# Optimization experiments

Hardware: AMD Instinct MI355X
Metric: run time of the kernel (lower is better)

## Reference

```python
import jax, jax.numpy as jnp
import numpy as np

N = 40000      # nodes
E = 640000     # edges (avg degree 16)
H = 128        # hidden_dim
D = 4          # propagation_depth
G = 1250       # graphs in batch
T = 32         # target_dim
AF, AV = 9, 64   # atom categorical features, vocab per feature
BF, BV = 3, 8    # bond categorical features, vocab per feature


def silu(x):
    return x * jax.nn.sigmoid(x)


def setup_inputs() -> dict:
    key = jax.random.key(0)
    ks = jax.random.split(key, 32)
    s = 1.0 / np.sqrt(H)

    def w(i, shp, scale):
        return (jax.random.normal(ks[i], shp, jnp.float32) * scale).astype(jnp.float32)

    inp = {}
    inp["atom_feat"] = jax.random.randint(ks[0], (N, AF), 0, AV)
    inp["bond_feat"] = jax.random.randint(ks[1], (E, BF), 0, BV)
    inp["edge_src"] = jax.random.randint(ks[2], (E,), 0, N)
    inp["edge_dst"] = jax.random.randint(ks[3], (E,), 0, N)
    inp["node2graph"] = jnp.sort(jax.random.randint(ks[4], (N,), 0, G))

    inp["atom_emb"] = w(5, (AF, AV, H), 0.1)
    inp["bond_emb"] = w(6, (BF, BV, H), 0.1)
    # message MLP: Linear(3H,H)+SiLU, Linear(H,H)+SiLU (last_activation=mid_activation)
    inp["msg_W1"] = w(7, (D, 3 * H, H), 1.0 / np.sqrt(3 * H))
    inp["msg_b1"] = jnp.zeros((D, H), jnp.float32)
    inp["msg_W2"] = w(8, (D, H, H), s)
    inp["msg_b2"] = jnp.zeros((D, H), jnp.float32)
    # soft edge gate: Linear(H,1) + sigmoid
    inp["gate_W"] = w(9, (D, H, 1), s)
    inp["gate_b"] = jnp.zeros((D, 1), jnp.float32)
    # update MLP: Linear(H,H)+SiLU, Linear(H,H) (last None)
    inp["upd_W1"] = w(10, (D, H, H), s)
    inp["upd_b1"] = jnp.zeros((D, H), jnp.float32)
    inp["upd_W2"] = w(11, (D, H, H), s)
    inp["upd_b2"] = jnp.zeros((D, H), jnp.float32)
    # node_wise_output: Linear(H,H)+SiLU, Linear(H,H) (last None)
    inp["out_W1"] = w(12, (H, H), s)
    inp["out_b1"] = jnp.zeros((H,), jnp.float32)
    inp["out_W2"] = w(13, (H, H), s)
    inp["out_b2"] = jnp.zeros((H,), jnp.float32)
    # readout output MLP: Linear(3H,H)+ReLU, Linear(H,T) (last None)
    inp["ro_W1"] = w(14, (3 * H, H), 1.0 / np.sqrt(3 * H))
    inp["ro_b1"] = jnp.zeros((H,), jnp.float32)
    inp["ro_W2"] = w(15, (H, T), s)
    inp["ro_b2"] = jnp.zeros((T,), jnp.float32)
    return inp


def _forward(atom_feat, bond_feat, edge_src, edge_dst, node2graph,
             atom_emb, bond_emb,
             msg_W1, msg_b1, msg_W2, msg_b2, gate_W, gate_b,
             upd_W1, upd_b1, upd_W2, upd_b2,
             out_W1, out_b1, out_W2, out_b2,
             ro_W1, ro_b1, ro_W2, ro_b2):
    # Atom/Bond encoders: sum of per-feature categorical embeddings
    h = atom_emb[jnp.arange(AF), atom_feat].sum(axis=1)        # [N, H]
    e = bond_emb[jnp.arange(BF), bond_feat].sum(axis=1)        # [E, H]

    for l in range(D):
        src = h[edge_src]                                      # [E, H]
        dst = h[edge_dst]                                      # [E, H]
        m_in = jnp.concatenate([src, dst, e], axis=-1)         # [E, 3H]
        m = silu(silu(m_in @ msg_W1[l] + msg_b1[l]) @ msg_W2[l] + msg_b2[l])
        gate = jax.nn.sigmoid(m @ gate_W[l] + gate_b[l])       # [E, 1]
        m = m * gate
        m_sum = jax.ops.segment_sum(m, edge_dst, num_segments=N)  # [N, H]
        u_in = m_sum + h
        h_new = silu(u_in @ upd_W1[l] + upd_b1[l]) @ upd_W2[l] + upd_b2[l]
        h = h_new + h

    # node-wise output network
    h = silu(h @ out_W1 + out_b1) @ out_W2 + out_b2            # [N, H]

    # per-graph readouts: sum / mean / max
    sums = jax.ops.segment_sum(h, node2graph, num_segments=G)  # [G, H]
    cnt = jax.ops.segment_sum(jnp.ones((N, 1), h.dtype), node2graph, num_segments=G)
    mean = sums / jnp.maximum(cnt, 1.0)
    mx = jax.ops.segment_max(h, node2graph, num_segments=G)
    mx = jnp.where(cnt > 0, mx, 0.0)
    readout = jnp.concatenate([sums, mean, mx], axis=-1)       # [G, 3H]

    return jax.nn.relu(readout @ ro_W1 + ro_b1) @ ro_W2 + ro_b2  # [G, T]


def reference(atom_feat, bond_feat, edge_src, edge_dst, node2graph,
              atom_emb, bond_emb,
              msg_W1, msg_b1, msg_W2, msg_b2, gate_W, gate_b,
              upd_W1, upd_b1, upd_W2, upd_b2,
              out_W1, out_b1, out_W2, out_b2,
              ro_W1, ro_b1, ro_W2, ro_b2):
    return _forward(atom_feat, bond_feat, edge_src, edge_dst, node2graph,
                    atom_emb, bond_emb,
                    msg_W1, msg_b1, msg_W2, msg_b2, gate_W, gate_b,
                    upd_W1, upd_b1, upd_W2, upd_b2,
                    out_W1, out_b1, out_W2, out_b2,
                    ro_W1, ro_b1, ro_W2, ro_b2)
```

## Files before the change

kernel.cpp:

```cpp
#include <hip/hip_runtime.h>
#include <hip/hip_bf16.h>

#define NN 40000
#define NE 640000
#define HD 128
#define DEPTH 4
#define NG 1250
#define TD 32
#define AFN 9
#define AVN 64
#define BFN 3
#define BVN 8
#define NBLK (NE / 64)

typedef short bf16x8 __attribute__((ext_vector_type(8)));
typedef float f32x4 __attribute__((ext_vector_type(4)));

__device__ __forceinline__ uint cvtpk(float lo, float hi){
  uint r; asm("v_cvt_pk_bf16_f32 %0, %1, %2" : "=v"(r) : "v"(lo), "v"(hi)); return r;
}
__device__ __forceinline__ ushort f2bf(float x){
  return (ushort)cvtpk(x, x);
}
__device__ __forceinline__ float bf2f(ushort b){ return __uint_as_float(((uint)b) << 16); }
__device__ __forceinline__ float lo16f(uint w){ return __uint_as_float(w << 16); }
__device__ __forceinline__ float hi16f(uint w){ return __uint_as_float(w & 0xffff0000u); }
__device__ __forceinline__ float rcpfa(float x){ return __builtin_amdgcn_rcpf(x); }
__device__ __forceinline__ float siluf(float x){ return x * rcpfa(1.f + __expf(-x)); }
__device__ __forceinline__ float sigmf(float x){ return rcpfa(1.f + __expf(-x)); }
__device__ __forceinline__ uint packbf2(float a, float b){ return cvtpk(a, b); }

__global__ void pack_w(const float* __restrict__ src, ushort* __restrict__ dst,
                       int K, int N, int L){
  int total = L * K * N;
  for (int idx = blockIdx.x * blockDim.x + threadIdx.x; idx < total;
       idx += gridDim.x * blockDim.x){
    int l = idx / (K * N);
    int r = idx - l * K * N;
    int k = r / N;
    int n = r - k * N;
    dst[(size_t)l * K * N + ((size_t)(k >> 3) * N + n) * 8 + (k & 7)] = f2bf(src[idx]);
  }
}

__global__ void zero_f(float4* __restrict__ p, int n4){
  for (int i = blockIdx.x * blockDim.x + threadIdx.x; i < n4; i += gridDim.x * blockDim.x)
    p[i] = make_float4(0.f, 0.f, 0.f, 0.f);
}

__global__ void zero_i(int* __restrict__ p, int n){
  for (int i = blockIdx.x * blockDim.x + threadIdx.x; i < n; i += gridDim.x * blockDim.x)
    p[i] = 0;
}

__global__ void atom_encode(const int* __restrict__ feat, const float* __restrict__ emb,
                            float* __restrict__ h, ushort* __restrict__ hbf){
  int n = blockIdx.x;
  int c = threadIdx.x;
  float acc = 0.f;
#pragma unroll
  for (int f = 0; f < AFN; ++f){
    int v = feat[n * AFN + f];
    acc += emb[(size_t)(f * AVN + v) * HD + c];
  }
  h[(size_t)n * HD + c] = acc;
  hbf[(size_t)n * HD + c] = f2bf(acc);
}

__global__ void ebf_k(const float* __restrict__ bemb, ushort* __restrict__ ebf){
  const int cid = blockIdx.x;
  const int c = threadIdx.x;
  const int f0 = cid >> 6, f1 = (cid >> 3) & 7, f2 = cid & 7;
  float v = bemb[(size_t)(0 * BVN + f0) * HD + c]
          + bemb[(size_t)(1 * BVN + f1) * HD + c]
          + bemb[(size_t)(2 * BVN + f2) * HD + c];
  ebf[(size_t)cid * HD + c] = f2bf(v);
}

__global__ void hist_k(const int* __restrict__ edst, int* __restrict__ deg){
  for (int e = blockIdx.x * blockDim.x + threadIdx.x; e < NE; e += gridDim.x * blockDim.x)
    atomicAdd(&deg[edst[e]], 1);
}

__global__ __launch_bounds__(1024) void scan_head(const int* __restrict__ deg,
                                                  int* __restrict__ head){
  __shared__ int buf[1024];
  const int t = threadIdx.x;
  const int base = t * 40;
  int s = 0;
  int dloc[40];
  if (t < 1000){
#pragma unroll
    for (int i = 0; i < 40; ++i){ dloc[i] = deg[base + i]; s += dloc[i]; }
  }
  buf[t] = s;
  __syncthreads();
  for (int ofs = 1; ofs < 1024; ofs <<= 1){
    int x = (t >= ofs) ? buf[t - ofs] : 0;
    __syncthreads();
    buf[t] += x;
    __syncthreads();
  }
  if (t < 1000){
    int run = buf[t] - s;
#pragma unroll
    for (int i = 0; i < 40; ++i){ head[base + i] = run; run += dloc[i]; }
  }
}

__global__ void scatter_k(const int* __restrict__ esrc, const int* __restrict__ edst,
                          const int* __restrict__ bfeat, int* __restrict__ head,
                          int* __restrict__ esrc_p, int* __restrict__ dst_p,
                          int* __restrict__ cid_p){
  for (int e = blockIdx.x * blockDim.x + threadIdx.x; e < NE; e += gridDim.x * blockDim.x){
    const int d = edst[e];
    const int pos = atomicAdd(&head[d], 1);
    esrc_p[pos] = esrc[e];
    dst_p[pos] = d;
    cid_p[pos] = bfeat[e * 3 + 0] * 64 + bfeat[e * 3 + 1] * 8 + bfeat[e * 3 + 2];
  }
}

__global__ __launch_bounds__(256) void pre_k(
    const ushort* __restrict__ hbf, const ushort* __restrict__ W1p,
    ushort* __restrict__ prea, ushort* __restrict__ preb)
{
  const int tid = threadIdx.x;
  const int n0 = blockIdx.x * 64;
  const int lane = tid & 63, wv = tid >> 6;
  const int lr = lane & 15, lg = lane >> 4;
  const int arow = n0 + wv * 16 + lr;
  bf16x8 a[4];
#pragma unroll
  for (int ks = 0; ks < 4; ++ks)
    a[ks] = *(const bf16x8*)(hbf + (size_t)arow * HD + ks * 32 + lg * 8);
  const f32x4 zero = {0.f, 0.f, 0.f, 0.f};
  f32x4 acc[16];
#pragma unroll
  for (int i = 0; i < 16; ++i) acc[i] = zero;
#pragma unroll
  for (int ks = 0; ks < 4; ++ks){
#pragma unroll
    for (int ct = 0; ct < 16; ++ct){
      const int oct = ks * 4 + lg + ((ct >= 8) ? 16 : 0);
      const int ncol = (ct & 7) * 16 + lr;
      bf16x8 b = *(const bf16x8*)(W1p + ((size_t)oct * HD + ncol) * 8);
      acc[ct] = __builtin_amdgcn_mfma_f32_16x16x32_bf16(a[ks], b, acc[ct], 0, 0, 0);
    }
  }
#pragma unroll
  for (int ct = 0; ct < 16; ++ct){
    ushort* dstp = (ct < 8) ? prea : preb;
    const int ncol = (ct & 7) * 16 + lr;
#pragma unroll
    for (int r = 0; r < 4; ++r){
      const int nrow = n0 + wv * 16 + lg * 4 + r;
      dstp[(size_t)nrow * HD + ncol] = f2bf(acc[ct][r]);
    }
  }
}

__global__ __launch_bounds__(256) void ew1c_k(
    const ushort* __restrict__ ebf, const ushort* __restrict__ W1p_all,
    const float* __restrict__ b1_all, ushort* __restrict__ ecb_all)
{
  const int l = blockIdx.y;
  const ushort* W1p = W1p_all + (size_t)l * 384 * HD;
  const float* b1v = b1_all + l * HD;
  ushort* ecb = ecb_all + (size_t)l * 512 * HD;
  const int tid = threadIdx.x;
  const int c0 = blockIdx.x * 64;
  const int lane = tid & 63, wv = tid >> 6;
  const int lr = lane & 15, lg = lane >> 4;
  const int arow = c0 + wv * 16 + lr;
  bf16x8 a[4];
#pragma unroll
  for (int ks = 0; ks < 4; ++ks)
    a[ks] = *(const bf16x8*)(ebf + (size_t)arow * HD + ks * 32 + lg * 8);
  const f32x4 zero = {0.f, 0.f, 0.f, 0.f};
  f32x4 acc[8];
#pragma unroll
  for (int i = 0; i < 8; ++i) acc[i] = zero;
#pragma unroll
  for (int ks = 0; ks < 4; ++ks){
#pragma unroll
    for (int ct = 0; ct < 8; ++ct){
      const int oct = ks * 4 + lg + 32;
      const int ncol = ct * 16 + lr;
      bf16x8 b = *(const bf16x8*)(W1p + ((size_t)oct * HD + ncol) * 8);
      acc[ct] = __builtin_amdgcn_mfma_f32_16x16x32_bf16(a[ks], b, acc[ct], 0, 0, 0);
    }
  }
#pragma unroll
  for (int ct = 0; ct < 8; ++ct){
    const int ncol = ct * 16 + lr;
    const float bias = b1v[ncol];
#pragma unroll
    for (int r = 0; r < 4; ++r){
      const int nrow = c0 + wv * 16 + lg * 4 + r;
      ecb[(size_t)nrow * HD + ncol] = f2bf(acc[ct][r] + bias);
    }
  }
}

__global__ __launch_bounds__(256, 4) void msg2_kernel(
    const ushort* __restrict__ prea, const ushort* __restrict__ preb,
    const ushort* __restrict__ ecb,
    const int* __restrict__ esrc_p, const int* __restrict__ dst_p,
    const int* __restrict__ cid_p,
    const ushort* __restrict__ W2p, const float* __restrict__ b2v,
    const float* __restrict__ gw, const float* __restrict__ gb,
    float* __restrict__ msum)
{
  __shared__ float Ms[64 * 128];
  __shared__ int dsh[64];
  const int tid = threadIdx.x;
  const int bid = (int)blockIdx.x;
  const int bsw = (bid & 7) * (NBLK >> 3) + (bid >> 3);
  const int e0 = bsw * 64;
  if (tid < 64) dsh[tid] = dst_p[e0 + tid];

  const int lane = tid & 63;
  const int wv = tid >> 6;
  const int lr = lane & 15, lg = lane >> 4;
  const int row = e0 + wv * 16 + lr;
  const int s = esrc_p[row];
  const int d = dst_p[row];
  const int c = cid_p[row];

  bf16x8 af[4];
#pragma unroll
  for (int ks = 0; ks < 4; ++ks){
    const int off = ks * 32 + lg * 8;
    union { bf16x8 v; uint u[4]; } ua, ub, uc, uo;
    ua.v = *(const bf16x8*)(prea + (size_t)s * HD + off);
    ub.v = *(const bf16x8*)(preb + (size_t)d * HD + off);
    uc.v = *(const bf16x8*)(ecb + (size_t)c * HD + off);
#pragma unroll
    for (int j = 0; j < 4; ++j){
      float xl = lo16f(ua.u[j]) + lo16f(ub.u[j]) + lo16f(uc.u[j]);
      float xh = hi16f(ua.u[j]) + hi16f(ub.u[j]) + hi16f(uc.u[j]);
      uo.u[j] = cvtpk(siluf(xl), siluf(xh));
    }
    af[ks] = uo.v;
  }

  const f32x4 zero = {0.f, 0.f, 0.f, 0.f};
  f32x4 acc[8];
#pragma unroll
  for (int i = 0; i < 8; ++i) acc[i] = zero;
#pragma unroll
  for (int ks = 0; ks < 4; ++ks){
    const ushort* wb = W2p + ((size_t)(ks * 4 + lg) * HD + lr) * 8;
#pragma unroll
    for (int ct = 0; ct < 8; ++ct){
      bf16x8 b = *(const bf16x8*)(wb + ct * 16 * 8);
      acc[ct] = __builtin_amdgcn_mfma_f32_16x16x32_bf16(af[ks], b, acc[ct], 0, 0, 0);
    }
  }

  float m[8][4];
#pragma unroll
  for (int ct = 0; ct < 8; ++ct){
    const float bias = b2v[ct * 16 + lr];
#pragma unroll
    for (int r = 0; r < 4; ++r) m[ct][r] = siluf(acc[ct][r] + bias);
  }
  float gwv[8];
#pragma unroll
  for (int ct = 0; ct < 8; ++ct) gwv[ct] = gw[ct * 16 + lr];
  const float gbias = gb[0];
#pragma unroll
  for (int r = 0; r < 4; ++r){
    float sgs = 0.f;
#pragma unroll
    for (int ct = 0; ct < 8; ++ct) sgs += m[ct][r] * gwv[ct];
    sgs += __shfl_xor(sgs, 1); sgs += __shfl_xor(sgs, 2);
    sgs += __shfl_xor(sgs, 4); sgs += __shfl_xor(sgs, 8);
    const float gate = sigmf(sgs + gbias);
#pragma unroll
    for (int ct = 0; ct < 8; ++ct) m[ct][r] *= gate;
  }

#pragma unroll
  for (int ct = 0; ct < 8; ++ct){
    const int col = ct * 16 + lr;
#pragma unroll
    for (int r = 0; r < 4; ++r){
      const int lrow = wv * 16 + lg * 4 + r;
      *(float*)((char*)Ms + lrow * 512 + (((uint)(col * 4)) ^ ((uint)((lrow & 7) << 4)))) = m[ct][r];
    }
  }
  __syncthreads();

  {
    const int col = tid & 127;
    const int seg = tid >> 7;
    const int r0 = seg * 32, r1 = r0 + 32;
    float run = 0.f;
    int cur = dsh[r0];
    for (int r = r0; r < r1; ++r){
      const int dd = dsh[r];
      if (dd != cur){
        atomicAdd(&msum[(size_t)cur * HD + col], run);
        run = 0.f; cur = dd;
      }
      run += *(const float*)((const char*)Ms + r * 512 +
                             (((uint)(col * 4)) ^ ((uint)((r & 7) << 4))));
    }
    atomicAdd(&msum[(size_t)cur * HD + col], run);
  }
}

template <int MODE>
__global__ __launch_bounds__(256) void node_mlp(
    const float* hin, const float* __restrict__ msum,
    const ushort* __restrict__ W1p, const ushort* __restrict__ W2p,
    const float* __restrict__ b1v, const float* __restrict__ b2v,
    float* outp, ushort* __restrict__ hbf)
{
  __shared__ ushort At[64 * 128];
  __shared__ ushort Tt[64 * 128];
  const int tid = threadIdx.x;
  const int n0 = blockIdx.x * 64;

  {
    const int nl = tid >> 2, part = tid & 3;
    const int node = n0 + nl;
    const float4* hp = (const float4*)(hin + (size_t)node * HD + part * 32);
    const float4* mp = (MODE == 0) ? (const float4*)(msum + (size_t)node * HD + part * 32) : nullptr;
    char* rowp = (char*)At + nl * 256;
    const uint sw = (uint)((nl & 7) << 4);
#pragma unroll
    for (int j = 0; j < 4; ++j){
      float4 x0 = hp[j * 2 + 0], x1 = hp[j * 2 + 1];
      if (MODE == 0){
        float4 m0 = mp[j * 2 + 0], m1 = mp[j * 2 + 1];
        x0.x += m0.x; x0.y += m0.y; x0.z += m0.z; x0.w += m0.w;
        x1.x += m1.x; x1.y += m1.y; x1.z += m1.z; x1.w += m1.w;
      }
      uint4 o;
      o.x = packbf2(x0.x, x0.y); o.y = packbf2(x0.z, x0.w);
      o.z = packbf2(x1.x, x1.y); o.w = packbf2(x1.z, x1.w);
      uint cb = (uint)(part * 64 + j * 16);
      *(uint4*)(rowp + (cb ^ sw)) = o;
    }
  }
  __syncthreads();

  const int lane = tid & 63;
  const int wv = tid >> 6;
  const int lr = lane & 15, lg = lane >> 4;
  const int rowbase = wv * 16;
  const f32x4 zero = {0.f, 0.f, 0.f, 0.f};

  f32x4 acc[8];
#pragma unroll
  for (int i = 0; i < 8; ++i) acc[i] = zero;
  {
    const int arow = rowbase + lr;
    const char* arp = (const char*)At + arow * 256;
    const uint asw = (uint)((arow & 7) << 4);
#pragma unroll
    for (int ks = 0; ks < 4; ++ks){
      uint cb = (uint)(ks * 64 + lg * 16);
      bf16x8 a = *(const bf16x8*)(arp + (cb ^ asw));
      const ushort* wbase = W1p + ((size_t)(ks * 4 + lg) * 128 + lr) * 8;
#pragma unroll
      for (int ct = 0; ct < 8; ++ct){
        bf16x8 b = *(const bf16x8*)(wbase + ct * 16 * 8);
        acc[ct] = __builtin_amdgcn_mfma_f32_16x16x32_bf16(a, b, acc[ct], 0, 0, 0);
      }
    }
  }
#pragma unroll
  for (int ct = 0; ct < 8; ++ct){
    const int col = ct * 16 + lr;
    const float bias = b1v[col];
#pragma unroll
    for (int r = 0; r < 4; ++r){
      const int row = rowbase + lg * 4 + r;
      float v = siluf(acc[ct][r] + bias);
      *(ushort*)((char*)Tt + row * 256 + (((uint)(col * 2)) ^ ((uint)(row & 7) << 4))) = f2bf(v);
    }
  }
  __syncthreads();

  f32x4 acc2[8];
#pragma unroll
  for (int i = 0; i < 8; ++i) acc2[i] = zero;
  {
    const int arow = rowbase + lr;
    const char* arp = (const char*)Tt + arow * 256;
    const uint asw = (uint)((arow & 7) << 4);
#pragma unroll
    for (int ks = 0; ks < 4; ++ks){
      uint cb = (uint)(ks * 64 + lg * 16);
      bf16x8 a = *(const bf16x8*)(arp + (cb ^ asw));
      const ushort* wbase = W2p + ((size_t)(ks * 4 + lg) * 128 + lr) * 8;
#pragma unroll
      for (int ct = 0; ct < 8; ++ct){
        bf16x8 b = *(const bf16x8*)(wbase + ct * 16 * 8);
        acc2[ct] = __builtin_amdgcn_mfma_f32_16x16x32_bf16(a, b, acc2[ct], 0, 0, 0);
      }
    }
  }
#pragma unroll
  for (int ct = 0; ct < 8; ++ct){
    const int col = ct * 16 + lr;
    const float bias = b2v[col];
#pragma unroll
    for (int r = 0; r < 4; ++r){
      const int node = n0 + rowbase + lg * 4 + r;
      float v = acc2[ct][r] + bias;
      if (MODE == 0) v += hin[(size_t)node * HD + col];
      outp[(size_t)node * HD + col] = v;
      if (MODE == 0) hbf[(size_t)node * HD + col] = f2bf(v);
    }
  }
}

__global__ void readout_k(const float* __restrict__ hout, const int* __restrict__ n2g,
                          float* __restrict__ ro){
  const int g = blockIdx.x;
  const int c = threadIdx.x;
  int lo, hi;
  { int a = 0, b = NN; while (a < b){ int mid = (a + b) >> 1; if (n2g[mid] < g) a = mid + 1; else b = mid; } lo = a; }
  { int a = lo, b = NN; while (a < b){ int mid = (a + b) >> 1; if (n2g[mid] < g + 1) a = mid + 1; else b = mid; } hi = a; }
  float s = 0.f, mx = -3.4e38f;
  for (int n = lo; n < hi; ++n){
    float v = hout[(size_t)n * HD + c];
    s += v; mx = fmaxf(mx, v);
  }
  const int cnt = hi - lo;
  float mean = (cnt > 0) ? s / (float)cnt : 0.f;
  if (cnt == 0){ s = 0.f; mx = 0.f; }
  ro[(size_t)g * 384 + c] = s;
  ro[(size_t)g * 384 + 128 + c] = mean;
  ro[(size_t)g * 384 + 256 + c] = mx;
}

__global__ void final_k(const float* __restrict__ ro,
                        const float* __restrict__ W1, const float* __restrict__ b1,
                        const float* __restrict__ W2, const float* __restrict__ b2,
                        float* __restrict__ out){
  __shared__ float rsh[384];
  __shared__ float hr[128];
  const int g = blockIdx.x;
  const int t = threadIdx.x;
  for (int i = t; i < 384; i += 128) rsh[i] = ro[(size_t)g * 384 + i];
  __syncthreads();
  float acc = b1[t];
#pragma unroll 4
  for (int j = 0; j < 384; ++j) acc += rsh[j] * W1[j * 128 + t];
  hr[t] = fmaxf(acc, 0.f);
  __syncthreads();
  if (t < TD){
    float o = b2[t];
#pragma unroll 4
    for (int j = 0; j < 128; ++j) o += hr[j] * W2[j * TD + t];
    out[(size_t)g * TD + t] = o;
  }
}

extern "C" void kernel_launch(void* const* d_in, const int* in_sizes, int n_in,
                              void* d_out, int out_size, void* d_ws, size_t ws_size,
                              hipStream_t stream)
{
  const int*   atom_feat  = (const int*)  d_in[0];
  const int*   bond_feat  = (const int*)  d_in[1];
  const int*   edge_src   = (const int*)  d_in[2];
  const int*   edge_dst   = (const int*)  d_in[3];
  const int*   node2graph = (const int*)  d_in[4];
  const float* atom_emb   = (const float*)d_in[5];
  const float* bond_emb   = (const float*)d_in[6];
  const float* msg_W1     = (const float*)d_in[7];
  const float* msg_b1     = (const float*)d_in[8];
  const float* msg_W2     = (const float*)d_in[9];
  const float* msg_b2     = (const float*)d_in[10];
  const float* gate_W     = (const float*)d_in[11];
  const float* gate_b     = (const float*)d_in[12];
  const float* upd_W1     = (const float*)d_in[13];
  const float* upd_b1     = (const float*)d_in[14];
  const float* upd_W2     = (const float*)d_in[15];
  const float* upd_b2     = (const float*)d_in[16];
  const float* out_W1     = (const float*)d_in[17];
  const float* out_b1     = (const float*)d_in[18];
  const float* out_W2     = (const float*)d_in[19];
  const float* out_b2     = (const float*)d_in[20];
  const float* ro_W1      = (const float*)d_in[21];
  const float* ro_b1      = (const float*)d_in[22];
  const float* ro_W2      = (const float*)d_in[23];
  const float* ro_b2      = (const float*)d_in[24];
  (void)in_sizes; (void)n_in; (void)out_size; (void)ws_size;

  char* ws = (char*)d_ws;
  size_t off = 0;
  auto alloc = [&](size_t bytes) -> char* {
    char* p = ws + off;
    off = (off + bytes + 255) & ~(size_t)255;
    return p;
  };
  float*  h      = (float*) alloc((size_t)NN * HD * 4);
  ushort* hbf    = (ushort*)alloc((size_t)NN * HD * 2);
  float*  msum   = (float*) alloc((size_t)NN * HD * 4);
  float*  ro     = (float*) alloc((size_t)NG * 3 * HD * 4);
  ushort* msgW1p = (ushort*)alloc((size_t)DEPTH * 384 * HD * 2);
  ushort* msgW2p = (ushort*)alloc((size_t)DEPTH * HD * HD * 2);
  ushort* updW1p = (ushort*)alloc((size_t)DEPTH * HD * HD * 2);
  ushort* updW2p = (ushort*)alloc((size_t)DEPTH * HD * HD * 2);
  ushort* outW1p = (ushort*)alloc((size_t)HD * HD * 2);
  ushort* outW2p = (ushort*)alloc((size_t)HD * HD * 2);
  ushort* ebf    = (ushort*)alloc((size_t)512 * HD * 2);
  ushort* ecb    = (ushort*)alloc((size_t)DEPTH * 512 * HD * 2);
  ushort* prea   = (ushort*)alloc((size_t)NN * HD * 2);
  ushort* preb   = (ushort*)alloc((size_t)NN * HD * 2);
  int*    deg    = (int*)   alloc((size_t)NN * 4);
  int*    head   = (int*)   alloc((size_t)NN * 4);
  int*    esrc_p = (int*)   alloc((size_t)NE * 4);
  int*    dst_p  = (int*)   alloc((size_t)NE * 4);
  int*    cid_p  = (int*)   alloc((size_t)NE * 4);
  float*  hout   = msum;

  pack_w<<<192, 256, 0, stream>>>(msg_W1, msgW1p, 384, HD, DEPTH);
  pack_w<<<64, 256, 0, stream>>>(msg_W2, msgW2p, HD, HD, DEPTH);
  pack_w<<<64, 256, 0, stream>>>(upd_W1, updW1p, HD, HD, DEPTH);
  pack_w<<<64, 256, 0, stream>>>(upd_W2, updW2p, HD, HD, DEPTH);
  pack_w<<<32, 256, 0, stream>>>(out_W1, outW1p, HD, HD, 1);
  pack_w<<<32, 256, 0, stream>>>(out_W2, outW2p, HD, HD, 1);
  atom_encode<<<NN, HD, 0, stream>>>(atom_feat, atom_emb, h, hbf);
  ebf_k<<<512, HD, 0, stream>>>(bond_emb, ebf);
  ew1c_k<<<dim3(8, DEPTH), 256, 0, stream>>>(ebf, msgW1p, msg_b1, ecb);

  zero_i<<<160, 256, 0, stream>>>(deg, NN);
  hist_k<<<640, 256, 0, stream>>>(edge_dst, deg);
  scan_head<<<1, 1024, 0, stream>>>(deg, head);
  scatter_k<<<640, 256, 0, stream>>>(edge_src, edge_dst, bond_feat, head,
                                     esrc_p, dst_p, cid_p);

  for (int l = 0; l < DEPTH; ++l){
    pre_k<<<NN / 64, 256, 0, stream>>>(hbf, msgW1p + (size_t)l * 384 * HD, prea, preb);
    zero_f<<<1024, 256, 0, stream>>>((float4*)msum, NN * HD / 4);
    msg2_kernel<<<NBLK, 256, 0, stream>>>(
        prea, preb, ecb + (size_t)l * 512 * HD,
        esrc_p, dst_p, cid_p,
        msgW2p + (size_t)l * HD * HD,
        msg_b2 + l * HD, gate_W + l * HD, gate_b + l, msum);
    node_mlp<0><<<NN / 64, 256, 0, stream>>>(
        h, msum,
        updW1p + (size_t)l * HD * HD, updW2p + (size_t)l * HD * HD,
        upd_b1 + l * HD, upd_b2 + l * HD, h, hbf);
  }
  node_mlp<1><<<NN / 64, 256, 0, stream>>>(
      h, nullptr, outW1p, outW2p, out_b1, out_b2, hout, nullptr);
  readout_k<<<NG, HD, 0, stream>>>(hout, node2graph, ro);
  final_k<<<NG, HD, 0, stream>>>(ro, ro_W1, ro_b1, ro_W2, ro_b2, (float*)d_out);
}
```

Before: 785.6 us.

## Fuse next-layer pre-projection into node MLP and pack message tile as bf16

The per-layer pre_k projection (h @ W1 slices for src/dst) is moved into the tail of node_mlp, computed from the freshly updated h still held in shared memory. This removes the separate kernel launch and the hbf write and read-back each layer. The msg2 shared staging buffer now holds messages packed as bf16 pairs, which halves LDS use, and launch bounds rise to 6 blocks per CU. Segment sums are accumulated from bf16-rounded messages, which adds precision loss before the atomics, and the extra MFMA work in node_mlp may raise register pressure there.

```diff
diff --git a/kernel.cpp b/kernel.cpp
--- a/kernel.cpp
+++ b/kernel.cpp
@@ -203,7 +203,7 @@
   }
 }
 
-__global__ __launch_bounds__(256, 4) void msg2_kernel(
+__global__ __launch_bounds__(256, 6) void msg2_kernel(
     const ushort* __restrict__ prea, const ushort* __restrict__ preb,
     const ushort* __restrict__ ecb,
     const int* __restrict__ esrc_p, const int* __restrict__ dst_p,
@@ -212,7 +212,7 @@
     const float* __restrict__ gw, const float* __restrict__ gb,
     float* __restrict__ msum)
 {
-  __shared__ float Ms[64 * 128];
+  __shared__ uint Ms[64 * 64];
   __shared__ int dsh[64];
   const int tid = threadIdx.x;
   const int bid = (int)blockIdx.x;
@@ -283,41 +283,46 @@
   }
 
 #pragma unroll
-  for (int ct = 0; ct < 8; ++ct){
-    const int col = ct * 16 + lr;
+  for (int ct = 0; ct < 4; ++ct){
+    const int ui = ct * 16 + lr;
 #pragma unroll
     for (int r = 0; r < 4; ++r){
       const int lrow = wv * 16 + lg * 4 + r;
-      *(float*)((char*)Ms + lrow * 512 + (((uint)(col * 4)) ^ ((uint)((lrow & 7) << 4)))) = m[ct][r];
+      *(uint*)((char*)Ms + lrow * 256 + (((uint)(ui * 4)) ^ ((uint)((lrow & 7) << 4)))) =
+          cvtpk(m[ct][r], m[ct + 4][r]);
     }
   }
   __syncthreads();
 
   {
-    const int col = tid & 127;
-    const int seg = tid >> 7;
-    const int r0 = seg * 32, r1 = r0 + 32;
-    float run = 0.f;
+    const int cp = tid & 63;
+    const int seg = tid >> 6;
+    const int r0 = seg * 16, r1 = r0 + 16;
+    float rl = 0.f, rh = 0.f;
     int cur = dsh[r0];
     for (int r = r0; r < r1; ++r){
       const int dd = dsh[r];
       if (dd != cur){
-        atomicAdd(&msum[(size_t)cur * HD + col], run);
-        run = 0.f; cur = dd;
+        atomicAdd(&msum[(size_t)cur * HD + cp], rl);
+        atomicAdd(&msum[(size_t)cur * HD + cp + 64], rh);
+        rl = 0.f; rh = 0.f; cur = dd;
       }
-      run += *(const float*)((const char*)Ms + r * 512 +
-                             (((uint)(col * 4)) ^ ((uint)((r & 7) << 4))));
-    }
-    atomicAdd(&msum[(size_t)cur * HD + col], run);
-  }
-}
-
-template <int MODE>
+      uint w = *(const uint*)((const char*)Ms + r * 256 +
+                              (((uint)(cp * 4)) ^ ((uint)((r & 7) << 4))));
+      rl += lo16f(w); rh += hi16f(w);
+    }
+    atomicAdd(&msum[(size_t)cur * HD + cp], rl);
+    atomicAdd(&msum[(size_t)cur * HD + cp + 64], rh);
+  }
+}
+
+template <int MODE, int DO_PRE>
 __global__ __launch_bounds__(256) void node_mlp(
     const float* hin, const float* __restrict__ msum,
     const ushort* __restrict__ W1p, const ushort* __restrict__ W2p,
     const float* __restrict__ b1v, const float* __restrict__ b2v,
-    float* outp, ushort* __restrict__ hbf)
+    float* outp,
+    const ushort* __restrict__ W1n, ushort* __restrict__ prea, ushort* __restrict__ preb)
 {
   __shared__ ushort At[64 * 128];
   __shared__ ushort Tt[64 * 128];
@@ -353,24 +358,22 @@
   const int lr = lane & 15, lg = lane >> 4;
   const int rowbase = wv * 16;
   const f32x4 zero = {0.f, 0.f, 0.f, 0.f};
+  const int arow = rowbase + lr;
+  const char* arp = (const char*)At + arow * 256;
+  const uint asw = (uint)((arow & 7) << 4);
 
   f32x4 acc[8];
 #pragma unroll
   for (int i = 0; i < 8; ++i) acc[i] = zero;
-  {
-    const int arow = rowbase + lr;
-    const char* arp = (const char*)At + arow * 256;
-    const uint asw = (uint)((arow & 7) << 4);
-#pragma unroll
-    for (int ks = 0; ks < 4; ++ks){
-      uint cb = (uint)(ks * 64 + lg * 16);
-      bf16x8 a = *(const bf16x8*)(arp + (cb ^ asw));
-      const ushort* wbase = W1p + ((size_t)(ks * 4 + lg) * 128 + lr) * 8;
-#pragma unroll
-      for (int ct = 0; ct < 8; ++ct){
-        bf16x8 b = *(const bf16x8*)(wbase + ct * 16 * 8);
-        acc[ct] = __builtin_amdgcn_mfma_f32_16x16x32_bf16(a, b, acc[ct], 0, 0, 0);
-      }
+#pragma unroll
+  for (int ks = 0; ks < 4; ++ks){
+    uint cb = (uint)(ks * 64 + lg * 16);
+    bf16x8 a = *(const bf16x8*)(arp + (cb ^ asw));
+    const ushort* wbase = W1p + ((size_t)(ks * 4 + lg) * 128 + lr) * 8;
+#pragma unroll
+    for (int ct = 0; ct < 8; ++ct){
+      bf16x8 b = *(const bf16x8*)(wbase + ct * 16 * 8);
+      acc[ct] = __builtin_amdgcn_mfma_f32_16x16x32_bf16(a, b, acc[ct], 0, 0, 0);
     }
   }
 #pragma unroll
@@ -390,13 +393,11 @@
 #pragma unroll
   for (int i = 0; i < 8; ++i) acc2[i] = zero;
   {
-    const int arow = rowbase + lr;
-    const char* arp = (const char*)Tt + arow * 256;
-    const uint asw = (uint)((arow & 7) << 4);
+    const char* trp = (const char*)Tt + arow * 256;
 #pragma unroll
     for (int ks = 0; ks < 4; ++ks){
       uint cb = (uint)(ks * 64 + lg * 16);
-      bf16x8 a = *(const bf16x8*)(arp + (cb ^ asw));
+      bf16x8 a = *(const bf16x8*)(trp + (cb ^ asw));
       const ushort* wbase = W2p + ((size_t)(ks * 4 + lg) * 128 + lr) * 8;
 #pragma unroll
       for (int ct = 0; ct < 8; ++ct){
@@ -415,7 +416,44 @@
       float v = acc2[ct][r] + bias;
       if (MODE == 0) v += hin[(size_t)node * HD + col];
       outp[(size_t)node * HD + col] = v;
-      if (MODE == 0) hbf[(size_t)node * HD + col] = f2bf(v);
+      if (DO_PRE){
+        const int row = rowbase + lg * 4 + r;
+        *(ushort*)((char*)At + row * 256 + (((uint)(col * 2)) ^ ((uint)((row & 7) << 4)))) = f2bf(v);
+      }
+    }
+  }
+  if (DO_PRE){
+    __syncthreads();
+    bf16x8 a[4];
+#pragma unroll
+    for (int ks = 0; ks < 4; ++ks){
+      uint cb = (uint)(ks * 64 + lg * 16);
+      a[ks] = *(const bf16x8*)(arp + (cb ^ asw));
+    }
+#pragma unroll
+    for (int p = 0; p < 2; ++p){
+      f32x4 pacc[8];
+#pragma unroll
+      for (int i = 0; i < 8; ++i) pacc[i] = zero;
+#pragma unroll
+      for (int ks = 0; ks < 4; ++ks){
+        const ushort* wbase = W1n + ((size_t)((ks * 4 + lg) + p * 16) * 128 + lr) * 8;
+#pragma unroll
+        for (int ct = 0; ct < 8; ++ct){
+          bf16x8 b = *(const bf16x8*)(wbase + ct * 16 * 8);
+          pacc[ct] = __builtin_amdgcn_mfma_f32_16x16x32_bf16(a[ks], b, pacc[ct], 0, 0, 0);
+        }
+      }
+      ushort* dstp = p ? preb : prea;
+#pragma unroll
+      for (int ct = 0; ct < 8; ++ct){
+        const int ncol = ct * 16 + lr;
+#pragma unroll
+        for (int r = 0; r < 4; ++r){
+          const int nrow = n0 + rowbase + lg * 4 + r;
+          dstp[(size_t)nrow * HD + ncol] = f2bf(pacc[ct][r]);
+        }
+      }
     }
   }
 }
@@ -538,21 +576,31 @@
   scatter_k<<<640, 256, 0, stream>>>(edge_src, edge_dst, bond_feat, head,
                                      esrc_p, dst_p, cid_p);
 
+  pre_k<<<NN / 64, 256, 0, stream>>>(hbf, msgW1p, prea, preb);
+
   for (int l = 0; l < DEPTH; ++l){
-    pre_k<<<NN / 64, 256, 0, stream>>>(hbf, msgW1p + (size_t)l * 384 * HD, prea, preb);
     zero_f<<<1024, 256, 0, stream>>>((float4*)msum, NN * HD / 4);
     msg2_kernel<<<NBLK, 256, 0, stream>>>(
         prea, preb, ecb + (size_t)l * 512 * HD,
         esrc_p, dst_p, cid_p,
         msgW2p + (size_t)l * HD * HD,
         msg_b2 + l * HD, gate_W + l * HD, gate_b + l, msum);
-    node_mlp<0><<<NN / 64, 256, 0, stream>>>(
-        h, msum,
-        updW1p + (size_t)l * HD * HD, updW2p + (size_t)l * HD * HD,
-        upd_b1 + l * HD, upd_b2 + l * HD, h, hbf);
-  }
-  node_mlp<1><<<NN / 64, 256, 0, stream>>>(
-      h, nullptr, outW1p, outW2p, out_b1, out_b2, hout, nullptr);
+    if (l < DEPTH - 1){
+      node_mlp<0, 1><<<NN / 64, 256, 0, stream>>>(
+          h, msum,
+          updW1p + (size_t)l * HD * HD, updW2p + (size_t)l * HD * HD,
+          upd_b1 + l * HD, upd_b2 + l * HD, h,
+          msgW1p + (size_t)(l + 1) * 384 * HD, prea, preb);
+    } else {
+      node_mlp<0, 0><<<NN / 64, 256, 0, stream>>>(
+          h, msum,
+          updW1p + (size_t)l * HD * HD, updW2p + (size_t)l * HD * HD,
+          upd_b1 + l * HD, upd_b2 + l * HD, h,
+          nullptr, nullptr, nullptr);
+    }
+  }
+  node_mlp<1, 0><<<NN / 64, 256, 0, stream>>>(
+      h, nullptr, outW1p, outW2p, out_b1, out_b2, hout, nullptr, nullptr, nullptr);
   readout_k<<<NG, HD, 0, stream>>>(hout, node2graph, ro);
   final_k<<<NG, HD, 0, stream>>>(ro, ro_W1, ro_b1, ro_W2, ro_b2, (float*)d_out);
 }
```

Measured after the change: 797.8 us. Within noise of the previous version (+1.5%).
